# Kernel optimization log

Measured on AMD Instinct MI355X. Metric: run time of the kernel, lower is better.

Reference implementation:

```python
import jax, jax.numpy as jnp
from jax import lax
import numpy as np

N_HEAD = 16
KERNEL = 3
ROPE_BASE = 10000.0


def _rope_tables(T, D, dtype):
    inv_freq = 1.0 / (ROPE_BASE ** (jnp.arange(0, D, 2, dtype=jnp.float32) / D))
    t = jnp.arange(T, dtype=jnp.float32)
    freqs = t[:, None] * inv_freq[None, :]           # [T, D/2]
    emb = jnp.concatenate([freqs, freqs], axis=-1)   # [T, D]
    return jnp.cos(emb).astype(dtype), jnp.sin(emb).astype(dtype)


def _rotate_half(x):
    x1, x2 = jnp.split(x, 2, axis=-1)
    return jnp.concatenate([-x2, x1], axis=-1)


def setup_inputs() -> dict:
    key = jax.random.key(0)
    k1, k2, k3, k4 = jax.random.split(key, 4)
    B, T, C = 2, 2048, 2048
    s = 0.02
    return {
        "x": jax.random.normal(k1, (B, T, C), dtype=jnp.float32),
        "conv_w": jax.random.normal(k2, (C, 1, KERNEL), dtype=jnp.float32) * s,
        "w_attn": jax.random.normal(k3, (3 * C, C), dtype=jnp.float32) * s,
        "w_proj": jax.random.normal(k4, (C, C), dtype=jnp.float32) * s,
    }


def reference(x, conv_w, w_attn, w_proj):
    B, T, C = x.shape
    H = N_HEAD
    D = C // H

    # causal depthwise conv1d: left-pad K-1, groups=C
    xc = jnp.transpose(x, (0, 2, 1))                       # [B, C, T]
    xc = jnp.pad(xc, ((0, 0), (0, 0), (KERNEL - 1, 0)))
    xc = lax.conv_general_dilated(
        xc, conv_w, window_strides=(1,), padding="VALID",
        feature_group_count=C, dimension_numbers=("NCH", "OIH", "NCH"))
    xconv = jnp.transpose(xc, (0, 2, 1))                   # [B, T, C]

    # fused QKV projection
    qkv = xconv @ w_attn.T                                 # [B, T, 3C]
    q, k, v = jnp.split(qkv, 3, axis=-1)
    q = q.reshape(B, T, H, D)
    k = k.reshape(B, T, H, D)
    v = v.reshape(B, T, H, D)

    # rotary embedding
    cos, sin = _rope_tables(T, D, x.dtype)                 # [T, D]
    cos = cos[None, :, None, :]
    sin = sin[None, :, None, :]
    q = q * cos + _rotate_half(q) * sin
    k = k * cos + _rotate_half(k) * sin

    # causal SDPA
    scale = 1.0 / jnp.sqrt(jnp.asarray(D, dtype=x.dtype))
    scores = jnp.einsum("bthd,bshd->bhts", q, k) * scale   # [B, H, T, T]
    causal = jnp.tril(jnp.ones((T, T), dtype=bool))
    scores = jnp.where(causal[None, None], scores, jnp.finfo(scores.dtype).min)
    p = jax.nn.softmax(scores, axis=-1)
    y = jnp.einsum("bhts,bshd->bthd", p, v).reshape(B, T, C)

    return y @ w_proj.T
```

## Files before the change

kernel.cpp:

```cpp
#include <hip/hip_runtime.h>

typedef __attribute__((ext_vector_type(8))) short bf16x8;
typedef __attribute__((ext_vector_type(4))) float f32x4;
typedef __attribute__((ext_vector_type(4))) unsigned short u16x4;

#define DEV static __device__ __forceinline__

DEV float bf2f(unsigned short u) {
  union { unsigned int i; float f; } v; v.i = ((unsigned int)u) << 16; return v.f;
}
DEV unsigned short f2bf(float f) {
  unsigned int x = __float_as_uint(f);
  x += 0x7fffu + ((x >> 16) & 1u);
  return (unsigned short)(x >> 16);
}
DEV f32x4 mfma16(bf16x8 a, bf16x8 b, f32x4 c) {
  return __builtin_amdgcn_mfma_f32_16x16x32_bf16(a, b, c, 0, 0, 0);
}
DEV void gload_lds16(const void* g, void* l) {
  __builtin_amdgcn_global_load_lds(
      (const __attribute__((address_space(1))) unsigned int*)g,
      (__attribute__((address_space(3))) unsigned int*)l, 16, 0, 0);
}

__global__ void build_tables(float* __restrict__ ct, float* __restrict__ st) {
  int idx = blockIdx.x * 256 + threadIdx.x;
  int i = idx & 63, t = idx >> 6;
  float f = powf(10000.0f, -(float)i * (1.0f / 64.0f));
  float a = (float)t * f;
  ct[idx] = cosf(a);
  st[idx] = sinf(a);
}

__global__ void cast_bf(const float* __restrict__ in, unsigned short* __restrict__ out, int n4) {
  int idx = blockIdx.x * 256 + threadIdx.x;
  if (idx >= n4) return;
  f32x4 v = *(const f32x4*)(in + (size_t)idx * 4);
  u16x4 o;
  #pragma unroll
  for (int j = 0; j < 4; ++j) o[j] = f2bf(v[j]);
  *(u16x4*)(out + (size_t)idx * 4) = o;
}

__global__ void conv_cast(const float* __restrict__ x, const float* __restrict__ w,
                          unsigned short* __restrict__ out) {
  int idx = blockIdx.x * 256 + threadIdx.x;
  int c4 = idx & 511, t = (idx >> 9) & 2047;
  int c = c4 * 4;
  const float* xp = x + (size_t)(idx >> 20) * 2048 * 2048 + (size_t)t * 2048 + c;
  f32x4 v2 = *(const f32x4*)xp;
  f32x4 v1 = {0.f, 0.f, 0.f, 0.f}, v0 = {0.f, 0.f, 0.f, 0.f};
  if (t >= 1) v1 = *(const f32x4*)(xp - 2048);
  if (t >= 2) v0 = *(const f32x4*)(xp - 4096);
  u16x4 o;
  #pragma unroll
  for (int j = 0; j < 4; ++j) {
    float val = v0[j] * w[(c + j) * 3 + 0] + v1[j] * w[(c + j) * 3 + 1] + v2[j] * w[(c + j) * 3 + 2];
    o[j] = f2bf(val);
  }
  *(u16x4*)(idx * 4 + out) = o;
}

template <int MFRAG, int NFRAG, bool OUT_BF16>
__global__ __launch_bounds__(512, 2) void gemm2p(const unsigned short* __restrict__ A,
                                                 const unsigned short* __restrict__ Bw,
                                                 void* __restrict__ Cp, int M, int N, int K) {
  constexpr int BM = MFRAG * 32;
  constexpr int BN = NFRAG * 64;
  constexpr int ALD = BM / 128;
  constexpr int BLD = BN / 128;
  constexpr int STEADY = 2 * (ALD + BLD);
  constexpr int HALF = ALD + BLD;
  __shared__ __align__(16) unsigned short As[2][2][BM * 32];
  __shared__ __align__(16) unsigned short Bs[2][2][BN * 32];
  const int tid = threadIdx.x;
  const int w = tid >> 6, l = tid & 63;
  const int lr = l & 15, lg = l >> 4;
  const int wm = w >> 2, wn = w & 3;
  const int nbx = N / BN, nby = M / BM;
  const int nwg = nbx * nby;
  const int bid = blockIdx.x;
  const int wg = (bid & 7) * (nwg >> 3) + (bid >> 3);
  const int bx = wg / nby, by = wg % nby;
  const int m0 = by * BM, n0 = bx * BN;

  int aOff[ALD], bOff[BLD];
  #pragma unroll
  for (int it = 0; it < ALD; ++it) {
    int q = it * 512 + tid, row = q >> 2, cp = q & 3;
    aOff[it] = (m0 + row) * K + ((cp ^ ((row >> 1) & 3)) * 8);
  }
  #pragma unroll
  for (int it = 0; it < BLD; ++it) {
    int q = it * 512 + tid, row = q >> 2, cp = q & 3;
    bOff[it] = (n0 + row) * K + ((cp ^ ((row >> 1) & 3)) * 8);
  }
  const int dstW = w * 512;

  int aRd[MFRAG], bRd[NFRAG];
  #pragma unroll
  for (int m = 0; m < MFRAG; ++m) {
    int R = wm * (MFRAG * 16) + m * 16 + lr;
    aRd[m] = R * 32 + ((lg ^ ((R >> 1) & 3)) * 8);
  }
  #pragma unroll
  for (int n = 0; n < NFRAG; ++n) {
    int R = wn * (NFRAG * 16) + n * 16 + lr;
    bRd[n] = R * 32 + ((lg ^ ((R >> 1) & 3)) * 8);
  }

  auto stageA = [&](int tt, int kh) {
    const unsigned short* s = A + (size_t)(tt * 64 + kh * 32);
    unsigned short* d = (unsigned short*)As[tt & 1][kh] + dstW;
    #pragma unroll
    for (int it = 0; it < ALD; ++it) gload_lds16(s + aOff[it], d + it * 4096);
  };
  auto stageB = [&](int tt, int kh) {
    const unsigned short* s = Bw + (size_t)(tt * 64 + kh * 32);
    unsigned short* d = (unsigned short*)Bs[tt & 1][kh] + dstW;
    #pragma unroll
    for (int it = 0; it < BLD; ++it) gload_lds16(s + bOff[it], d + it * 4096);
  };
  #define WAIT_STEADY do { if constexpr (STEADY == 8) asm volatile("s_waitcnt vmcnt(8)" ::: "memory"); \
                           else asm volatile("s_waitcnt vmcnt(6)" ::: "memory"); } while (0)
  #define WAIT_HALF   do { if constexpr (HALF == 4) asm volatile("s_waitcnt vmcnt(4)" ::: "memory"); \
                           else asm volatile("s_waitcnt vmcnt(3)" ::: "memory"); } while (0)
  #define WAIT_ZERO   asm volatile("s_waitcnt vmcnt(0)" ::: "memory")

  #define PH(BUF, KH, STAGE_STMT, WAIT_STMT)                              \
  {                                                                       \
    const unsigned short* Ab = (const unsigned short*)As[BUF][KH];        \
    const unsigned short* Bb = (const unsigned short*)Bs[BUF][KH];        \
    bf16x8 aF[MFRAG], bF[NFRAG];                                          \
    _Pragma("unroll") for (int m = 0; m < MFRAG; ++m)                     \
        aF[m] = *(const bf16x8*)(Ab + aRd[m]);                            \
    _Pragma("unroll") for (int n = 0; n < NFRAG; ++n)                     \
        bF[n] = *(const bf16x8*)(Bb + bRd[n]);                            \
    STAGE_STMT;                                                           \
    __builtin_amdgcn_sched_barrier(0);                                    \
    __builtin_amdgcn_s_barrier();                                         \
    __builtin_amdgcn_sched_barrier(0);                                    \
    __builtin_amdgcn_s_setprio(1);                                        \
    _Pragma("unroll") for (int m = 0; m < MFRAG; ++m)                     \
      _Pragma("unroll") for (int n = 0; n < NFRAG; ++n)                   \
          acc[m][n] = mfma16(aF[m], bF[n], acc[m][n]);                    \
    __builtin_amdgcn_s_setprio(0);                                        \
    WAIT_STMT;                                                            \
    __builtin_amdgcn_sched_barrier(0);                                    \
    __builtin_amdgcn_s_barrier();                                         \
    __builtin_amdgcn_sched_barrier(0);                                    \
  }

  f32x4 acc[MFRAG][NFRAG] = {};
  const int NT = K >> 6;
  stageA(0, 0); stageB(0, 0);
  stageA(0, 1); stageB(0, 1);
  stageA(1, 0); stageB(1, 0);
  __builtin_amdgcn_sched_barrier(0);
  WAIT_STEADY;
  __builtin_amdgcn_s_barrier();
  __builtin_amdgcn_sched_barrier(0);

  int t = 0;
  for (; t + 2 < NT; ++t) {
    PH(t & 1, 0, { stageA(t + 1, 1); stageB(t + 1, 1); }, WAIT_STEADY);
    PH(t & 1, 1, { stageA(t + 2, 0); stageB(t + 2, 0); }, WAIT_STEADY);
  }
  PH(t & 1, 0, { stageA(t + 1, 1); stageB(t + 1, 1); }, WAIT_STEADY);
  PH(t & 1, 1, {}, WAIT_HALF);
  ++t;
  PH(t & 1, 0, {}, WAIT_ZERO);
  PH(t & 1, 1, {}, {});
  #undef PH
  #undef WAIT_STEADY
  #undef WAIT_HALF
  #undef WAIT_ZERO

  #pragma unroll
  for (int m = 0; m < MFRAG; ++m)
    #pragma unroll
    for (int r = 0; r < 4; ++r) {
      int row = m0 + wm * (MFRAG * 16) + m * 16 + lg * 4 + r;
      #pragma unroll
      for (int n = 0; n < NFRAG; ++n) {
        int col = n0 + wn * (NFRAG * 16) + n * 16 + lr;
        if (OUT_BF16) ((unsigned short*)Cp)[(size_t)row * N + col] = f2bf(acc[m][n][r]);
        else          ((float*)Cp)[(size_t)row * N + col] = acc[m][n][r];
      }
    }
}

__global__ __launch_bounds__(256) void rope_vt(const unsigned short* __restrict__ qkv,
                                               const float* __restrict__ ct,
                                               const float* __restrict__ st,
                                               unsigned short* __restrict__ Qo,
                                               unsigned short* __restrict__ Ko,
                                               unsigned short* __restrict__ Vt) {
  __shared__ unsigned short tile[64][136];
  const int bh = blockIdx.x, tt = blockIdx.y;
  const int b = bh >> 4, h = bh & 15;
  const unsigned short* base = qkv + ((size_t)(b * 2048 + tt * 64)) * 6144 + h * 128;
  {
    const int r = threadIdx.x >> 2, ch = threadIdx.x & 3;
    const unsigned short* vsrc = base + 4096 + (size_t)r * 6144;
    #pragma unroll
    for (int it = 0; it < 4; ++it) {
      int d0 = (ch * 4 + it) * 8;
      *(bf16x8*)&tile[r][d0] = *(const bf16x8*)(vsrc + d0);
    }
  }
  {
    const int i = threadIdx.x & 63, rr = threadIdx.x >> 6;
    #pragma unroll
    for (int jj = 0; jj < 16; ++jj) {
      int r = rr * 16 + jj;
      int t = tt * 64 + r;
      const unsigned short* src = base + (size_t)r * 6144;
      float cz = ct[t * 64 + i], sz = st[t * 64 + i];
      float q1 = bf2f(src[i]),        q2 = bf2f(src[i + 64]);
      float k1 = bf2f(src[2048 + i]), k2 = bf2f(src[2048 + i + 64]);
      size_t o = ((size_t)bh * 2048 + t) * 128 + i;
      Qo[o]      = f2bf(q1 * cz - q2 * sz);
      Qo[o + 64] = f2bf(q2 * cz + q1 * sz);
      Ko[o]      = f2bf(k1 * cz - k2 * sz);
      Ko[o + 64] = f2bf(k2 * cz + k1 * sz);
    }
  }
  __syncthreads();
  {
    const int d = threadIdx.x >> 1, half = threadIdx.x & 1;
    unsigned short* dst = Vt + ((size_t)bh * 128 + d) * 2048 + tt * 64;
    #pragma unroll
    for (int it = 0; it < 4; ++it) {
      int t0 = half * 32 + it * 8;
      bf16x8 v;
      #pragma unroll
      for (int j = 0; j < 8; ++j) ((unsigned short*)&v)[j] = tile[t0 + j][d];
      *(bf16x8*)(dst + t0) = v;
    }
  }
}

__global__ __launch_bounds__(256, 4) void attn_fwd(const unsigned short* __restrict__ Q,
                                                   const unsigned short* __restrict__ K,
                                                   const unsigned short* __restrict__ Vt,
                                                   unsigned short* __restrict__ Y) {
  const int T = 2048, D = 128, C = 2048;
  __shared__ __align__(16) unsigned short Ks[64 * 128];
  __shared__ __align__(16) unsigned short Vs[128 * 64];
  __shared__ __align__(16) unsigned short Pl[4][16 * 64];
  const int tid = threadIdx.x;
  const int w = tid >> 6, l = tid & 63;
  const int lr = l & 15, lg = l >> 4;
  const int bh = blockIdx.x;
  const int qi = (int)gridDim.y - 1 - (int)blockIdx.y;
  const int qbase = qi * 64;
  const size_t base = (size_t)bh * T * D;

  bf16x8 qf[4];
  {
    const unsigned short* qp = Q + base + (size_t)(qbase + w * 16 + lr) * D + lg * 8;
    #pragma unroll
    for (int d = 0; d < 4; ++d) qf[d] = *(const bf16x8*)(qp + d * 32);
  }
  int kSrc[4], vSrc[4], ldsDst[4];
  #pragma unroll
  for (int it = 0; it < 4; ++it) {
    int c = it * 256 + tid;
    int krow = c >> 4, kdc = c & 15;
    kSrc[it] = krow * D + ((kdc ^ (krow & 7)) * 8);
    int vd = c >> 3, vcc = c & 7;
    vSrc[it] = vd * T + ((vcc ^ (vd & 7)) * 8);
    ldsDst[it] = (it * 256 + w * 64) * 8;
  }
  f32x4 ao[8] = {};
  float mrun = -3.0e38f, lrun = 0.0f;
  const float cs = 0.08838834764831845f * 1.4426950408889634f;
  const float THR = 8.0f / cs;
  const int q_abs = qbase + w * 16 + lr;

  for (int kt = 0; kt <= qi; ++kt) {
    const int kv0 = kt * 64;
    #pragma unroll
    for (int it = 0; it < 4; ++it) {
      gload_lds16(K + base + (size_t)kv0 * D + kSrc[it], Ks + ldsDst[it]);
      gload_lds16(Vt + base + kv0 + vSrc[it], Vs + ldsDst[it]);
    }
    __syncthreads();
    f32x4 s4[4] = {};
    __builtin_amdgcn_s_setprio(1);
    #pragma unroll
    for (int n = 0; n < 4; ++n) {
      int row = n * 16 + lr;
      #pragma unroll
      for (int d = 0; d < 4; ++d) {
        bf16x8 kf = *(const bf16x8*)(Ks + row * 128 + (((d * 4 + lg) ^ (lr & 7)) * 8));
        s4[n] = mfma16(kf, qf[d], s4[n]);
      }
    }
    __builtin_amdgcn_s_setprio(0);
    if (kt == qi) {
      #pragma unroll
      for (int n = 0; n < 4; ++n)
        #pragma unroll
        for (int r = 0; r < 4; ++r)
          if (kv0 + n * 16 + lg * 4 + r > q_abs) s4[n][r] = -3.0e38f;
    }
    float mx = -3.0e38f;
    #pragma unroll
    for (int n = 0; n < 4; ++n)
      #pragma unroll
      for (int r = 0; r < 4; ++r) mx = fmaxf(mx, s4[n][r]);
    mx = fmaxf(mx, __shfl_xor(mx, 16, 64));
    mx = fmaxf(mx, __shfl_xor(mx, 32, 64));
    if (!__all(mx - mrun <= THR)) {
      float mnew = fmaxf(mrun, mx);
      float fac = exp2f((mrun - mnew) * cs);
      mrun = mnew;
      lrun *= fac;
      float fr[4];
      #pragma unroll
      for (int r = 0; r < 4; ++r) fr[r] = __shfl(fac, (l & 48) | (lg * 4 + r), 64);
      #pragma unroll
      for (int n8 = 0; n8 < 8; ++n8)
        #pragma unroll
        for (int r = 0; r < 4; ++r) ao[n8][r] *= fr[r];
    }
    float sum = 0.0f;
    #pragma unroll
    for (int n = 0; n < 4; ++n)
      #pragma unroll
      for (int r = 0; r < 4; ++r) {
        float p = exp2f((s4[n][r] - mrun) * cs);
        s4[n][r] = p;
        sum += p;
      }
    sum += __shfl_xor(sum, 16, 64);
    sum += __shfl_xor(sum, 32, 64);
    lrun += sum;
    unsigned short* pw = (unsigned short*)Pl[w];
    #pragma unroll
    for (int n = 0; n < 4; ++n)
      #pragma unroll
      for (int i = 0; i < 2; ++i) {
        unsigned int pk = (unsigned int)f2bf(s4[n][2 * i]) |
                          ((unsigned int)f2bf(s4[n][2 * i + 1]) << 16);
        int kv = n * 16 + lg * 4 + 2 * i;
        *(unsigned int*)(pw + lr * 64 + (((kv >> 3) ^ (lr & 7)) * 8) + (kv & 7)) = pk;
      }
    __builtin_amdgcn_s_setprio(1);
    #pragma unroll
    for (int ks = 0; ks < 2; ++ks) {
      bf16x8 pa = *(const bf16x8*)(pw + lr * 64 + (((ks * 4 + lg) ^ (lr & 7)) * 8));
      #pragma unroll
      for (int n = 0; n < 8; ++n) {
        int row = n * 16 + lr;
        bf16x8 vb = *(const bf16x8*)(Vs + row * 64 + (((ks * 4 + lg) ^ (lr & 7)) * 8));
        ao[n] = mfma16(pa, vb, ao[n]);
      }
    }
    __builtin_amdgcn_s_setprio(0);
    __syncthreads();
  }
  const int b = bh >> 4, h = bh & 15;
  #pragma unroll
  for (int r = 0; r < 4; ++r) {
    float lsum = __shfl(lrun, (l & 48) | (lg * 4 + r), 64);
    float inv = 1.0f / lsum;
    int t = qbase + w * 16 + lg * 4 + r;
    unsigned short* dst = Y + ((size_t)b * T + t) * C + h * D;
    #pragma unroll
    for (int n = 0; n < 8; ++n) dst[n * 16 + lr] = f2bf(ao[n][r] * inv);
  }
}

extern "C" void kernel_launch(void* const* d_in, const int* in_sizes, int n_in,
                              void* d_out, int out_size, void* d_ws, size_t ws_size,
                              hipStream_t stream) {
  const float* x      = (const float*)d_in[0];
  const float* conv_w = (const float*)d_in[1];
  const float* w_attn = (const float*)d_in[2];
  const float* w_proj = (const float*)d_in[3];
  float* out = (float*)d_out;
  char* ws = (char*)d_ws;

  unsigned short* qkv  = (unsigned short*)(ws);
  unsigned short* qb   = (unsigned short*)(ws + 50331648);
  unsigned short* kb   = (unsigned short*)(ws + 67108864);
  unsigned short* vt   = (unsigned short*)(ws + 83886080);
  unsigned short* xcy  = (unsigned short*)(ws + 100663296);
  unsigned short* wbuf = (unsigned short*)(ws + 117440512);
  float* ctab = (float*)(ws + 142606336);
  float* stab = (float*)(ws + 143130624);

  build_tables<<<512, 256, 0, stream>>>(ctab, stab);
  cast_bf<<<12288, 256, 0, stream>>>(w_attn, wbuf, 3145728);
  conv_cast<<<8192, 256, 0, stream>>>(x, conv_w, xcy);
  gemm2p<8, 4, true><<<384, 512, 0, stream>>>(xcy, wbuf, (void*)qkv, 4096, 6144, 2048);
  rope_vt<<<dim3(32, 32), 256, 0, stream>>>(qkv, ctab, stab, qb, kb, vt);
  cast_bf<<<4096, 256, 0, stream>>>(w_proj, wbuf, 1048576);
  attn_fwd<<<dim3(32, 32), 256, 0, stream>>>(qb, kb, vt, xcy);
  gemm2p<4, 4, false><<<256, 512, 0, stream>>>(xcy, wbuf, (void*)out, 4096, 2048, 2048);
}
```

Baseline: 289.2 us.

## Fuse RoPE and V transpose into QKV GEMM epilogue via LDS staging

The separate rope_vt kernel is removed. The QKV GEMM now stages its 256x256 output tile in shared memory (reusing the pipeline buffers with an XOR swizzle), applies rotary embedding for Q/K sections and writes the transposed V directly. This avoids writing and re-reading the full bf16 qkv intermediate and one kernel launch. In exchange the GEMM epilogue gets longer, with an extra sync and strided LDS reads for the V transpose.

Result: faster. 278.2 us, median of 2 (-3.8%).

```diff
diff --git a/kernel.cpp b/kernel.cpp
--- a/kernel.cpp
+++ b/kernel.cpp
@@ -61,18 +61,24 @@
   *(u16x4*)(idx * 4 + out) = o;
 }
 
-template <int MFRAG, int NFRAG, bool OUT_BF16>
+template <int MFRAG, int NFRAG, int MODE>
 __global__ __launch_bounds__(512, 2) void gemm2p(const unsigned short* __restrict__ A,
                                                  const unsigned short* __restrict__ Bw,
-                                                 void* __restrict__ Cp, int M, int N, int K) {
+                                                 void* __restrict__ Cp, int M, int N, int K,
+                                                 const float* __restrict__ ct,
+                                                 const float* __restrict__ st,
+                                                 unsigned short* __restrict__ Qo,
+                                                 unsigned short* __restrict__ Ko,
+                                                 unsigned short* __restrict__ Vt) {
   constexpr int BM = MFRAG * 32;
   constexpr int BN = NFRAG * 64;
   constexpr int ALD = BM / 128;
   constexpr int BLD = BN / 128;
   constexpr int STEADY = 2 * (ALD + BLD);
   constexpr int HALF = ALD + BLD;
-  __shared__ __align__(16) unsigned short As[2][2][BM * 32];
-  __shared__ __align__(16) unsigned short Bs[2][2][BN * 32];
+  __shared__ __align__(16) unsigned short smem[2 * 2 * (BM + BN) * 32];
+  unsigned short* AsB = smem;
+  unsigned short* BsB = smem + 2 * 2 * BM * 32;
   const int tid = threadIdx.x;
   const int w = tid >> 6, l = tid & 63;
   const int lr = l & 15, lg = l >> 4;
@@ -111,13 +117,13 @@
 
   auto stageA = [&](int tt, int kh) {
     const unsigned short* s = A + (size_t)(tt * 64 + kh * 32);
-    unsigned short* d = (unsigned short*)As[tt & 1][kh] + dstW;
+    unsigned short* d = AsB + ((tt & 1) * 2 + kh) * (BM * 32) + dstW;
     #pragma unroll
     for (int it = 0; it < ALD; ++it) gload_lds16(s + aOff[it], d + it * 4096);
   };
   auto stageB = [&](int tt, int kh) {
     const unsigned short* s = Bw + (size_t)(tt * 64 + kh * 32);
-    unsigned short* d = (unsigned short*)Bs[tt & 1][kh] + dstW;
+    unsigned short* d = BsB + ((tt & 1) * 2 + kh) * (BN * 32) + dstW;
     #pragma unroll
     for (int it = 0; it < BLD; ++it) gload_lds16(s + bOff[it], d + it * 4096);
   };
@@ -129,8 +135,8 @@
 
   #define PH(BUF, KH, STAGE_STMT, WAIT_STMT)                              \
   {                                                                       \
-    const unsigned short* Ab = (const unsigned short*)As[BUF][KH];        \
-    const unsigned short* Bb = (const unsigned short*)Bs[BUF][KH];        \
+    const unsigned short* Ab = AsB + ((BUF) * 2 + (KH)) * (BM * 32);      \
+    const unsigned short* Bb = BsB + ((BUF) * 2 + (KH)) * (BN * 32);      \
     bf16x8 aF[MFRAG], bF[NFRAG];                                          \
     _Pragma("unroll") for (int m = 0; m < MFRAG; ++m)                     \
         aF[m] = *(const bf16x8*)(Ab + aRd[m]);                            \
@@ -176,67 +182,78 @@
   #undef WAIT_HALF
   #undef WAIT_ZERO
 
-  #pragma unroll
-  for (int m = 0; m < MFRAG; ++m)
-    #pragma unroll
-    for (int r = 0; r < 4; ++r) {
-      int row = m0 + wm * (MFRAG * 16) + m * 16 + lg * 4 + r;
-      #pragma unroll
-      for (int n = 0; n < NFRAG; ++n) {
-        int col = n0 + wn * (NFRAG * 16) + n * 16 + lr;
-        if (OUT_BF16) ((unsigned short*)Cp)[(size_t)row * N + col] = f2bf(acc[m][n][r]);
-        else          ((float*)Cp)[(size_t)row * N + col] = acc[m][n][r];
-      }
-    }
-}
-
-__global__ __launch_bounds__(256) void rope_vt(const unsigned short* __restrict__ qkv,
-                                               const float* __restrict__ ct,
-                                               const float* __restrict__ st,
-                                               unsigned short* __restrict__ Qo,
-                                               unsigned short* __restrict__ Ko,
-                                               unsigned short* __restrict__ Vt) {
-  __shared__ unsigned short tile[64][136];
-  const int bh = blockIdx.x, tt = blockIdx.y;
-  const int b = bh >> 4, h = bh & 15;
-  const unsigned short* base = qkv + ((size_t)(b * 2048 + tt * 64)) * 6144 + h * 128;
-  {
-    const int r = threadIdx.x >> 2, ch = threadIdx.x & 3;
-    const unsigned short* vsrc = base + 4096 + (size_t)r * 6144;
-    #pragma unroll
-    for (int it = 0; it < 4; ++it) {
-      int d0 = (ch * 4 + it) * 8;
-      *(bf16x8*)&tile[r][d0] = *(const bf16x8*)(vsrc + d0);
-    }
-  }
-  {
-    const int i = threadIdx.x & 63, rr = threadIdx.x >> 6;
-    #pragma unroll
-    for (int jj = 0; jj < 16; ++jj) {
-      int r = rr * 16 + jj;
-      int t = tt * 64 + r;
-      const unsigned short* src = base + (size_t)r * 6144;
-      float cz = ct[t * 64 + i], sz = st[t * 64 + i];
-      float q1 = bf2f(src[i]),        q2 = bf2f(src[i + 64]);
-      float k1 = bf2f(src[2048 + i]), k2 = bf2f(src[2048 + i + 64]);
-      size_t o = ((size_t)bh * 2048 + t) * 128 + i;
-      Qo[o]      = f2bf(q1 * cz - q2 * sz);
-      Qo[o + 64] = f2bf(q2 * cz + q1 * sz);
-      Ko[o]      = f2bf(k1 * cz - k2 * sz);
-      Ko[o + 64] = f2bf(k2 * cz + k1 * sz);
-    }
-  }
-  __syncthreads();
-  {
-    const int d = threadIdx.x >> 1, half = threadIdx.x & 1;
-    unsigned short* dst = Vt + ((size_t)bh * 128 + d) * 2048 + tt * 64;
-    #pragma unroll
-    for (int it = 0; it < 4; ++it) {
-      int t0 = half * 32 + it * 8;
-      bf16x8 v;
-      #pragma unroll
-      for (int j = 0; j < 8; ++j) ((unsigned short*)&v)[j] = tile[t0 + j][d];
-      *(bf16x8*)(dst + t0) = v;
+  if constexpr (MODE == 0) {
+    #pragma unroll
+    for (int m = 0; m < MFRAG; ++m)
+      #pragma unroll
+      for (int r = 0; r < 4; ++r) {
+        int row = m0 + wm * (MFRAG * 16) + m * 16 + lg * 4 + r;
+        #pragma unroll
+        for (int n = 0; n < NFRAG; ++n) {
+          int col = n0 + wn * (NFRAG * 16) + n * 16 + lr;
+          ((float*)Cp)[(size_t)row * N + col] = acc[m][n][r];
+        }
+      }
+  } else {
+    static_assert(MODE != 1 || (BM == 256 && BN == 256), "fused epilogue needs 256x256");
+    auto tadr = [&](int row, int col) {
+      return row * 256 + ((((col >> 3) ^ (row & 7))) << 3) + (col & 7);
+    };
+    #pragma unroll
+    for (int m = 0; m < MFRAG; ++m)
+      #pragma unroll
+      for (int r = 0; r < 4; ++r) {
+        int row = wm * (MFRAG * 16) + m * 16 + lg * 4 + r;
+        #pragma unroll
+        for (int n = 0; n < NFRAG; ++n) {
+          int col = wn * (NFRAG * 16) + n * 16 + lr;
+          smem[tadr(row, col)] = f2bf(acc[m][n][r]);
+        }
+      }
+    __syncthreads();
+    const int sec = n0 >> 11;
+    const int hbase = (n0 & 2047) >> 7;
+    const int bb = m0 >> 11;
+    const int t0a = m0 & 2047;
+    if (sec < 2) {
+      unsigned short* outp = (sec == 0) ? Qo : Ko;
+      const int c8 = (tid & 31) * 8;
+      const int rb = tid >> 5;
+      const int dloc = c8 & 127;
+      const int hh = hbase + (c8 >> 7);
+      const bool lowh = dloc < 64;
+      const int ib = dloc & 63;
+      unsigned short* obase = outp + ((size_t)(bb * 16 + hh) * 2048) * 128;
+      #pragma unroll
+      for (int j = 0; j < 16; ++j) {
+        int row = rb * 16 + j;
+        int tt2 = t0a + row;
+        bf16x8 self = *(const bf16x8*)(smem + tadr(row, c8));
+        bf16x8 part = *(const bf16x8*)(smem + tadr(row, c8 ^ 64));
+        const float* cp2 = ct + tt2 * 64 + ib;
+        const float* sp2 = st + tt2 * 64 + ib;
+        bf16x8 o8;
+        #pragma unroll
+        for (int e = 0; e < 8; ++e) {
+          float a = bf2f(((const unsigned short*)&self)[e]);
+          float p = bf2f(((const unsigned short*)&part)[e]);
+          float cz = cp2[e], sz = sp2[e];
+          ((unsigned short*)&o8)[e] = f2bf(lowh ? (a * cz - p * sz) : (a * cz + p * sz));
+        }
+        *(bf16x8*)(obase + (size_t)tt2 * 128 + dloc) = o8;
+      }
+    } else {
+      const int c = tid >> 1, half = tid & 1;
+      const int dd = c & 127, hh = hbase + (c >> 7);
+      unsigned short* dst = Vt + ((size_t)(bb * 16 + hh) * 128 + dd) * 2048 + t0a + half * 128;
+      #pragma unroll
+      for (int j = 0; j < 16; ++j) {
+        bf16x8 v8;
+        #pragma unroll
+        for (int e = 0; e < 8; ++e)
+          ((unsigned short*)&v8)[e] = smem[tadr(half * 128 + j * 8 + e, c)];
+        *(bf16x8*)(dst + j * 8) = v8;
+      }
     }
   }
 }
@@ -384,7 +401,6 @@
   float* out = (float*)d_out;
   char* ws = (char*)d_ws;
 
-  unsigned short* qkv  = (unsigned short*)(ws);
   unsigned short* qb   = (unsigned short*)(ws + 50331648);
   unsigned short* kb   = (unsigned short*)(ws + 67108864);
   unsigned short* vt   = (unsigned short*)(ws + 83886080);
@@ -396,9 +412,10 @@
   build_tables<<<512, 256, 0, stream>>>(ctab, stab);
   cast_bf<<<12288, 256, 0, stream>>>(w_attn, wbuf, 3145728);
   conv_cast<<<8192, 256, 0, stream>>>(x, conv_w, xcy);
-  gemm2p<8, 4, true><<<384, 512, 0, stream>>>(xcy, wbuf, (void*)qkv, 4096, 6144, 2048);
-  rope_vt<<<dim3(32, 32), 256, 0, stream>>>(qkv, ctab, stab, qb, kb, vt);
+  gemm2p<8, 4, 1><<<384, 512, 0, stream>>>(xcy, wbuf, nullptr, 4096, 6144, 2048,
+                                           ctab, stab, qb, kb, vt);
   cast_bf<<<4096, 256, 0, stream>>>(w_proj, wbuf, 1048576);
   attn_fwd<<<dim3(32, 32), 256, 0, stream>>>(qb, kb, vt, xcy);
-  gemm2p<4, 4, false><<<256, 512, 0, stream>>>(xcy, wbuf, (void*)out, 4096, 2048, 2048);
-}
+  gemm2p<4, 4, 0><<<256, 512, 0, stream>>>(xcy, wbuf, (void*)out, 4096, 2048, 2048,
+                                           nullptr, nullptr, nullptr, nullptr, nullptr);
+}
```
